# Kernel tuning notes

Measured on AMD Instinct MI355X. Metric: run time of the kernel, lower is better.

Reference implementation:

```python
import jax, jax.numpy as jnp
import numpy as np

T = 1.0  # temperature

def _free_energy(v, W, b, c):
    # v: [B, V]; W: [V, H]; b: [V]; c: [H]
    vW = v @ W                                  # [B, H]
    W_colsum = W.sum(axis=0)                    # [H]
    negF_normal = (v * b).sum(-1) - jax.nn.softplus(vW + c).sum(-1)
    negF_flip = ((1.0 - v) * b).sum(-1) - jax.nn.softplus(W_colsum - vW + c).sum(-1)
    negF = jnp.stack([negF_normal, negF_flip], axis=-1)  # [B, 2]
    return -T * jax.nn.logsumexp(negF / T, axis=-1)      # [B]

def _gibbs_chain(v0, W, b, c, key, k):
    B = v0.shape[0]
    key, k0 = jax.random.split(key)
    u0 = jax.random.bernoulli(k0, 0.5, (B, 1)).astype(v0.dtype)
    b_sum = b.sum()

    def step(carry, _):
        v, u, key = carry
        key, k1, k2, k3 = jax.random.split(key, 4)
        v_branch = u * v + (1.0 - u) * (1.0 - v)
        h = jax.random.bernoulli(k1, jax.nn.sigmoid(v_branch @ W + c)).astype(v.dtype)  # [B,H]
        a = h @ W.T                                                                     # [B,V]
        vb = (v * b).sum(-1)
        va = (v * a).sum(-1)
        dE = -b_sum - a.sum(-1) + 2.0 * vb + 2.0 * va
        u_new = jax.random.bernoulli(k2, jax.nn.sigmoid(dE)).astype(v.dtype)[:, None]
        v_new = jax.random.bernoulli(k3, jax.nn.sigmoid(a + b)).astype(v.dtype)
        v = u_new * v_new + (1.0 - u_new) * (1.0 - v_new)
        return (v, u_new, key), None

    (v_model, _, _), _ = jax.lax.scan(step, (v0, u0, key), None, length=k)
    return v_model

def setup_inputs() -> dict:
    key = jax.random.key(0)
    kv, kw = jax.random.split(key)
    B, V, H = 8192, 1024, 1024
    v_data = jnp.round(jax.random.uniform(kv, (B, V), dtype=jnp.float32))  # binary 0/1
    W = 0.01 * jax.random.normal(kw, (V, H), dtype=jnp.float32)
    b = jnp.zeros((V,), dtype=jnp.float32)
    c = jnp.zeros((H,), dtype=jnp.float32)
    return {"v_data": v_data, "W": W, "b": b, "c": c, "seed": 0}

def reference(v_data, W, b, c, seed):
    K = 10  # Gibbs steps
    key = jax.random.key(seed)
    v_model = _gibbs_chain(v_data, W, b, c, key, K)
    v_model = jax.lax.stop_gradient(v_model)  # .detach() in torch
    loss = _free_energy(v_data, W, b, c).mean() - _free_energy(v_model, W, b, c).mean()
    return loss
```

## Files before the change

kernel.cpp:

```cpp
#include <hip/hip_runtime.h>
#include <hip/hip_bf16.h>
#include <stdint.h>
#include <math.h>


static constexpr int Bn = 8192;
static constexpr int Vn = 1024;
static constexpr int Hn = 1024;
static constexpr int KSTEPS = 10;

typedef _Float16 f16;
typedef f16   f16x4 __attribute__((ext_vector_type(4)));
typedef f16   f16x8 __attribute__((ext_vector_type(8)));
typedef float f32x4 __attribute__((ext_vector_type(4)));

#define GLOBAL_LOAD_LDS16(g, l)                                              \
  __builtin_amdgcn_global_load_lds(                                          \
      (const __attribute__((address_space(1))) uint32_t*)(g),                \
      (__attribute__((address_space(3))) uint32_t*)(l), 16, 0, 0)

__device__ __forceinline__ uint32_t rotl32(uint32_t x, int d) {
  return (x << d) | (x >> (32 - d));
}

__device__ __forceinline__ void tf2x32(uint32_t k0, uint32_t k1,
                                       uint32_t x0, uint32_t x1,
                                       uint32_t& o0, uint32_t& o1) {
  uint32_t k2 = k0 ^ k1 ^ 0x1BD11BDAu;
#define TFR(r) { x0 += x1; x1 = rotl32(x1, (r)); x1 ^= x0; }
  x0 += k0; x1 += k1;
  TFR(13) TFR(15) TFR(26) TFR(6)
  x0 += k1; x1 += k2 + 1u;
  TFR(17) TFR(29) TFR(16) TFR(24)
  x0 += k2; x1 += k0 + 2u;
  TFR(13) TFR(15) TFR(26) TFR(6)
  x0 += k0; x1 += k1 + 3u;
  TFR(17) TFR(29) TFR(16) TFR(24)
  x0 += k1; x1 += k2 + 4u;
  TFR(13) TFR(15) TFR(26) TFR(6)
  x0 += k2; x1 += k0 + 5u;
#undef TFR
  o0 = x0; o1 = x1;
}

__device__ __forceinline__ float rng_u01(uint2 key, uint32_t idx) {
  uint32_t o0, o1;
  tf2x32(key.x, key.y, 0u, idx, o0, o1);
  uint32_t bits = o0 ^ o1;
  return __uint_as_float((bits >> 9) | 0x3F800000u) - 1.0f;
}

__device__ __attribute__((noinline)) float4 rng4_u01(uint2 key, uint32_t i0,
                                                     uint32_t i1, uint32_t i2,
                                                     uint32_t i3) {
  float4 r;
  r.x = rng_u01(key, i0);
  r.y = rng_u01(key, i1);
  r.z = rng_u01(key, i2);
  r.w = rng_u01(key, i3);
  return r;
}

__device__ __forceinline__ float bern_fast(float z, float r01) {
  float e = __expf(-z);
  return (__builtin_fmaf(r01, e, r01) < 1.0f) ? 1.f : 0.f;
}
__device__ __forceinline__ float softplus_fast(float x) {
  return fmaxf(x, 0.f) + __logf(1.f + __expf(-fabsf(x)));
}

__global__ void prep_keys(const int* __restrict__ seedp, uint2* __restrict__ keys) {
  if (threadIdx.x != 0 || blockIdx.x != 0) return;
  uint32_t seed = (uint32_t)(*seedp);
  uint2 key = make_uint2(0u, seed);
  uint2 nk, kk;
  tf2x32(key.x, key.y, 0u, 0u, nk.x, nk.y);
  tf2x32(key.x, key.y, 0u, 1u, kk.x, kk.y);
  keys[0] = kk;
  key = nk;
  for (int s = 0; s < KSTEPS; ++s) {
    uint2 t0, t1, t2, t3;
    tf2x32(key.x, key.y, 0u, 0u, t0.x, t0.y);
    tf2x32(key.x, key.y, 0u, 1u, t1.x, t1.y);
    tf2x32(key.x, key.y, 0u, 2u, t2.x, t2.y);
    tf2x32(key.x, key.y, 0u, 3u, t3.x, t3.y);
    key = t0;
    keys[1 + 3*s] = t1;
    keys[2 + 3*s] = t2;
    keys[3 + 3*s] = t3;
  }
}

__global__ __launch_bounds__(256) void colsum_part(
    const float* __restrict__ W, float* __restrict__ part) {
  const int bx = blockIdx.x, t = threadIdx.x;
  float s0 = 0.f, s1 = 0.f, s2 = 0.f, s3 = 0.f;
#pragma unroll
  for (int r = 0; r < 16; ++r) {
    const float* row = W + (size_t)(bx * 16 + r) * Hn;
    s0 += row[t]; s1 += row[t + 256]; s2 += row[t + 512]; s3 += row[t + 768];
  }
  float* p = part + (size_t)bx * Hn;
  p[t] = s0; p[t + 256] = s1; p[t + 512] = s2; p[t + 768] = s3;
}

__global__ __launch_bounds__(256) void colsum_red(
    const float* __restrict__ part, float* __restrict__ cs) {
  const int col = blockIdx.x * 256 + threadIdx.x;
  float s = 0.f;
#pragma unroll
  for (int k = 0; k < 64; ++k) s += part[(size_t)k * Hn + col];
  cs[col] = s;
}

__global__ void bsum_k(const float* __restrict__ bvec, float* __restrict__ bs) {
  __shared__ float sb[4];
  float s = 0.f;
  for (int i = threadIdx.x; i < Vn; i += 256) s += bvec[i];
  for (int off = 32; off > 0; off >>= 1) s += __shfl_down(s, off, 64);
  int wv = threadIdx.x >> 6, ln = threadIdx.x & 63;
  if (ln == 0) sb[wv] = s;
  __syncthreads();
  if (threadIdx.x == 0) bs[0] = sb[0] + sb[1] + sb[2] + sb[3];
}

__global__ __launch_bounds__(256) void cast_W(
    const float* __restrict__ W, f16* __restrict__ Wf, f16* __restrict__ WTf) {
  __shared__ f16 tile[64][65];
  const int j0 = blockIdx.x * 64, i0 = blockIdx.y * 64;
  const int tx = threadIdx.x & 63, tg = threadIdx.x >> 6;
#pragma unroll 4
  for (int rr = 0; rr < 16; ++rr) {
    const int row = tg * 16 + rr;
    float w = W[(size_t)(i0 + row) * Hn + j0 + tx];
    f16 hw = (f16)w;
    Wf[(size_t)(i0 + row) * Hn + j0 + tx] = hw;
    tile[row][tx] = hw;
  }
  __syncthreads();
#pragma unroll 4
  for (int rr = 0; rr < 16; ++rr) {
    const int row = tg * 16 + rr;
    WTf[(size_t)(j0 + row) * Vn + i0 + tx] = tile[tx][row];
  }
}

__global__ void u0_init(const uint2* __restrict__ keys, float* __restrict__ u0) {
  int b = blockIdx.x * 256 + threadIdx.x;
  float r01 = rng_u01(keys[0], (uint32_t)b);
  u0[b] = (r01 < 0.5f) ? 1.f : 0.f;
}

__global__ __launch_bounds__(256) void cast_vx(
    const float* __restrict__ vd, const float* __restrict__ u0,
    const float* __restrict__ bvec, f16* __restrict__ x,
    float* __restrict__ pXB0) {
  const int row = blockIdx.x;
  const int t = threadIdx.x;
  const float uo = u0[row];
  const float4 d  = ((const float4*)(vd + (size_t)row * Vn))[t];
  const float4 bv = ((const float4*)bvec)[t];
  float xv[4] = { d.x, d.y, d.z, d.w };
  if (uo <= 0.5f) { xv[0]=1.f-xv[0]; xv[1]=1.f-xv[1]; xv[2]=1.f-xv[2]; xv[3]=1.f-xv[3]; }
  f16x4 o = { (f16)xv[0], (f16)xv[1], (f16)xv[2], (f16)xv[3] };
  *(f16x4*)(x + (size_t)row * Vn + t * 4) = o;
  float xb = xv[0]*bv.x + xv[1]*bv.y + xv[2]*bv.z + xv[3]*bv.w;
#pragma unroll
  for (int m = 1; m < 8; m <<= 1) xb += __shfl_xor(xb, m, 64);
  if ((t & 7) == 0) pXB0[(size_t)row * 32 + (t >> 3)] = xb;
}

template <int EPI>
__global__ __launch_bounds__(256, 2) void gemm_s(
    const f16* __restrict__ A, const f16* __restrict__ Bm,
    f16* __restrict__ outH, f16* __restrict__ xnew,
    const float* __restrict__ bvec, const float* __restrict__ cvec,
    const float* __restrict__ colsum,
    float* __restrict__ pA, float* __restrict__ pXA, float* __restrict__ pXBn,
    float* __restrict__ pSA, float* __restrict__ pSB,
    const uint2* __restrict__ keys, int keyIdx)
{
  constexpr int N = 1024, K = 1024, BK = 64;
  __shared__ alignas(16) f16 As[128 * BK];
  __shared__ alignas(16) f16 Bs[128 * BK];

  const int t = threadIdx.x, wave = t >> 6, lane = t & 63;
  const int l15 = lane & 15, quad = lane >> 4;
  const int m0 = blockIdx.x * 128, n0 = blockIdx.y * 128;
  const int wm = (wave >> 1) * 64, wn = (wave & 1) * 64;

  const int rbase = lane >> 3;
  const int gch   = (lane & 7) ^ rbase;
  const f16* gA = A  + (size_t)(m0 + wave * 32 + rbase) * K + gch * 8;
  const f16* gB = Bm + (size_t)(n0 + wave * 32 + rbase) * K + gch * 8;
  f16* lA = As + wave * 32 * BK;
  f16* lB = Bs + wave * 32 * BK;

  const int swz = l15 & 7;
  const int oA  = (wm + l15) * BK;
  const int oB  = (wn + l15) * BK;

  uint2 key = make_uint2(0u, 0u);
  if constexpr (EPI != 4) key = keys[keyIdx];

  f32x4 acc[4][4] = {};
  float r01v[64];

#pragma unroll 16
  for (int ki = 0; ki < 16; ++ki) {
    const int k0 = ki * 64;
#pragma unroll
    for (int i = 0; i < 4; ++i) {
      GLOBAL_LOAD_LDS16(gA + k0 + i * 8 * K, lA + i * 8 * BK);
      GLOBAL_LOAD_LDS16(gB + k0 + i * 8 * K, lB + i * 8 * BK);
    }
    if constexpr (EPI != 4) {
      uint32_t idx[4];
#pragma unroll
      for (int j = 0; j < 4; ++j) {
        const int e  = ki * 4 + j;
        const int mt = e >> 4, r = (e >> 2) & 3, nt = e & 3;
        const int gm = m0 + wm + mt * 16 + quad * 4 + r;
        const int gn = n0 + wn + nt * 16 + l15;
        idx[j] = (uint32_t)(gm * N + gn);
      }
      float4 rv = rng4_u01(key, idx[0], idx[1], idx[2], idx[3]);
      r01v[ki * 4 + 0] = rv.x;
      r01v[ki * 4 + 1] = rv.y;
      r01v[ki * 4 + 2] = rv.z;
      r01v[ki * 4 + 3] = rv.w;
    }
    __syncthreads();

#pragma unroll
    for (int kc = 0; kc < 2; ++kc) {
      const int fc = ((kc * 4 + quad) ^ swz) * 8;
      f16x8 af[4], bf[4];
#pragma unroll
      for (int i = 0; i < 4; ++i) {
        af[i] = *(const f16x8*)(&As[oA + i * 16 * BK + fc]);
        bf[i] = *(const f16x8*)(&Bs[oB + i * 16 * BK + fc]);
      }
#pragma unroll
      for (int mt = 0; mt < 4; ++mt)
#pragma unroll
        for (int nt = 0; nt < 4; ++nt)
          acc[mt][nt] = __builtin_amdgcn_mfma_f32_16x16x32_f16(af[mt], bf[nt], acc[mt][nt], 0, 0, 0);
    }
    __syncthreads();
  }

  const int slotBase = blockIdx.y * 4 + (wave & 1) * 2;

  if constexpr (EPI == 1 || EPI == 2) {
    float csv[4], cvv[4];
#pragma unroll
    for (int nt = 0; nt < 4; ++nt) {
      const int gn = n0 + wn + nt * 16 + l15;
      csv[nt] = colsum[gn];
      cvv[nt] = cvec[gn];
    }
#pragma unroll
    for (int mt = 0; mt < 4; ++mt)
#pragma unroll
      for (int r = 0; r < 4; ++r) {
        const int gm = m0 + wm + mt * 16 + quad * 4 + r;
#pragma unroll
        for (int p = 0; p < 2; ++p) {
          float pa = 0.f, pxa = 0.f, sa = 0.f, sb = 0.f;
#pragma unroll
          for (int q = 0; q < 2; ++q) {
            const int nt = p * 2 + q;
            const int gn = n0 + wn + nt * 16 + l15;
            const float val = acc[mt][nt][r];
            const float r01 = r01v[mt * 16 + r * 4 + nt];
            float hq  = bern_fast(val + cvv[nt], r01);
            outH[(size_t)gm * N + gn] = (f16)hq;
            pa  += hq * csv[nt];
            pxa += hq * val;
            if constexpr (EPI == 2) {
              sa += softplus_fast(val + cvv[nt]);
              sb += softplus_fast(csv[nt] - val + cvv[nt]);
            }
          }
#pragma unroll
          for (int m = 1; m < 16; m <<= 1) {
            pa  += __shfl_xor(pa,  m, 64);
            pxa += __shfl_xor(pxa, m, 64);
            if constexpr (EPI == 2) {
              sa += __shfl_xor(sa, m, 64);
              sb += __shfl_xor(sb, m, 64);
            }
          }
          if (l15 == 0) {
            pA [(size_t)gm * 32 + slotBase + p] = pa;
            pXA[(size_t)gm * 32 + slotBase + p] = pxa;
            if constexpr (EPI == 2) {
              pSA[(size_t)gm * 32 + slotBase + p] = sa;
              pSB[(size_t)gm * 32 + slotBase + p] = sb;
            }
          }
        }
      }
  } else if constexpr (EPI == 3) {
    float bb[4];
#pragma unroll
    for (int nt = 0; nt < 4; ++nt) bb[nt] = bvec[n0 + wn + nt * 16 + l15];
#pragma unroll
    for (int mt = 0; mt < 4; ++mt)
#pragma unroll
      for (int r = 0; r < 4; ++r) {
        const int gm = m0 + wm + mt * 16 + quad * 4 + r;
#pragma unroll
        for (int p = 0; p < 2; ++p) {
          float pxb = 0.f;
#pragma unroll
          for (int q = 0; q < 2; ++q) {
            const int nt = p * 2 + q;
            const int gn = n0 + wn + nt * 16 + l15;
            const float aval = acc[mt][nt][r];
            const float r01 = r01v[mt * 16 + r * 4 + nt];
            float xq  = bern_fast(aval + bb[nt], r01);
            xnew[(size_t)gm * N + gn] = (f16)xq;
            pxb += xq * bb[nt];
          }
#pragma unroll
          for (int m = 1; m < 16; m <<= 1) pxb += __shfl_xor(pxb, m, 64);
          if (l15 == 0) pXBn[(size_t)gm * 32 + slotBase + p] = pxb;
        }
      }
  } else {
    float csv[4], cvv[4];
#pragma unroll
    for (int nt = 0; nt < 4; ++nt) {
      const int gn = n0 + wn + nt * 16 + l15;
      csv[nt] = colsum[gn];
      cvv[nt] = cvec[gn];
    }
#pragma unroll
    for (int mt = 0; mt < 4; ++mt)
#pragma unroll
      for (int r = 0; r < 4; ++r) {
        const int gm = m0 + wm + mt * 16 + quad * 4 + r;
#pragma unroll
        for (int p = 0; p < 2; ++p) {
          float sa = 0.f, sb = 0.f;
#pragma unroll
          for (int q = 0; q < 2; ++q) {
            const int nt = p * 2 + q;
            const float val = acc[mt][nt][r];
            sa += softplus_fast(val + cvv[nt]);
            sb += softplus_fast(csv[nt] - val + cvv[nt]);
          }
#pragma unroll
          for (int m = 1; m < 16; m <<= 1) {
            sa += __shfl_xor(sa, m, 64);
            sb += __shfl_xor(sb, m, 64);
          }
          if (l15 == 0) {
            pSA[(size_t)gm * 32 + slotBase + p] = sa;
            pSB[(size_t)gm * 32 + slotBase + p] = sb;
          }
        }
      }
  }
}

__global__ __launch_bounds__(256) void u_chain(
    const float* __restrict__ pA, const float* __restrict__ pXA,
    const float* __restrict__ pXB, const float* __restrict__ bsum,
    const uint2* __restrict__ keys, const float* __restrict__ u0,
    float* __restrict__ uF)
{
  const int t = threadIdx.x, wave = t >> 6, lane = t & 63;
  const int r2 = lane >> 5, slot = lane & 31;
  const int row = blockIdx.x * 8 + wave * 2 + r2;
  const float bs = bsum[0];
  float uo = u0[row];
  for (int s = 0; s < KSTEPS; ++s) {
    const size_t o = (size_t)s * 32 * Bn + (size_t)row * 32 + slot;
    float sa  = pA [o];
    float sxa = pXA[o];
    float sxb = pXB[o];
#pragma unroll
    for (int m = 1; m < 32; m <<= 1) {
      sa  += __shfl_xor(sa,  m, 64);
      sxa += __shfl_xor(sxa, m, 64);
      sxb += __shfl_xor(sxb, m, 64);
    }
    const float va = (uo > 0.5f) ? sxa : sa - sxa;
    const float vb = (uo > 0.5f) ? sxb : bs - sxb;
    const float dE = -bs - sa + 2.f * vb + 2.f * va;
    uo = bern_fast(dE, rng_u01(keys[2 + 3 * s], (uint32_t)row));
  }
  if (slot == 0) uF[row] = uo;
}

__device__ __forceinline__ float fe_eval(float SA, float SB, float xb,
                                         float uo, float bs) {
  float S1 = (uo > 0.5f) ? SA : SB;
  float S2 = (uo > 0.5f) ? SB : SA;
  float vb = (uo > 0.5f) ? xb : bs - xb;
  float negn = vb - S1;
  float negf = (bs - vb) - S2;
  float mx = fmaxf(negn, negf);
  return -(mx + logf(expf(negn - mx) + expf(negf - mx)));
}

__global__ __launch_bounds__(256) void fe_finish(
    const float* __restrict__ SA0, const float* __restrict__ SB0,
    const float* __restrict__ xb0,
    const float* __restrict__ SAF, const float* __restrict__ SBF,
    const float* __restrict__ xbF,
    const float* __restrict__ u0, const float* __restrict__ uF,
    const float* __restrict__ bsum,
    float* __restrict__ Fd, float* __restrict__ Fm)
{
  const int t = threadIdx.x, wave = t >> 6, lane = t & 63;
  const int r2 = lane >> 5, slot = lane & 31;
  const int row = blockIdx.x * 8 + wave * 2 + r2;
  const size_t o = (size_t)row * 32 + slot;
  const float bs = bsum[0];
  float a0 = SA0[o], b0 = SB0[o], x0 = xb0[o];
  float aF = SAF[o], bF = SBF[o], xF = xbF[o];
#pragma unroll
  for (int m = 1; m < 32; m <<= 1) {
    a0 += __shfl_xor(a0, m, 64);  b0 += __shfl_xor(b0, m, 64);
    x0 += __shfl_xor(x0, m, 64);  aF += __shfl_xor(aF, m, 64);
    bF += __shfl_xor(bF, m, 64);  xF += __shfl_xor(xF, m, 64);
  }
  if (slot == 0) {
    Fd[row] = fe_eval(a0, b0, x0, u0[row], bs);
    Fm[row] = fe_eval(aF, bF, xF, uF[row], bs);
  }
}

__global__ __launch_bounds__(256) void finalize_k(
    const float* __restrict__ Fd, const float* __restrict__ Fm, float* __restrict__ out)
{
  __shared__ double sb[8];
  double sd = 0.0, sm = 0.0;
  for (int i = threadIdx.x; i < Bn; i += 256) { sd += (double)Fd[i]; sm += (double)Fm[i]; }
  for (int off = 32; off > 0; off >>= 1) { sd += __shfl_down(sd, off, 64); sm += __shfl_down(sm, off, 64); }
  const int wv = threadIdx.x >> 6, ln = threadIdx.x & 63;
  if (ln == 0) { sb[wv] = sd; sb[4 + wv] = sm; }
  __syncthreads();
  if (threadIdx.x == 0) {
    sd = sb[0] + sb[1] + sb[2] + sb[3];
    sm = sb[4] + sb[5] + sb[6] + sb[7];
    out[0] = (float)((sd - sm) / (double)Bn);
  }
}

extern "C" void kernel_launch(void* const* d_in, const int* in_sizes, int n_in,
                              void* d_out, int out_size, void* d_ws, size_t ws_size,
                              hipStream_t stream) {
  const float* v_data = (const float*)d_in[0];
  const float* W      = (const float*)d_in[1];
  const float* bvec   = (const float*)d_in[2];
  const float* cvec   = (const float*)d_in[3];
  const int*   seedp  = (const int*)d_in[4];
  float* out = (float*)d_out;

  char* ws = (char*)d_ws;
  size_t off = 0;
  auto alloc = [&](size_t bytes) -> void* {
    void* p = ws + off;
    off += (bytes + 255) & ~(size_t)255;
    return p;
  };
  f16*   xb0  = (f16*)alloc((size_t)Bn * Vn * 2);
  f16*   xb1  = (f16*)alloc((size_t)Bn * Vn * 2);
  f16*   h    = (f16*)alloc((size_t)Bn * Hn * 2);
  f16*   Wf   = (f16*)alloc((size_t)Vn * Hn * 2);
  f16*   WTf  = (f16*)alloc((size_t)Vn * Hn * 2);
  float* cpart  = (float*)alloc(64 * Hn * 4);
  float* colsum = (float*)alloc(Hn * 4);
  float* bsum   = (float*)alloc(256);
  uint2* keys   = (uint2*)alloc(64 * sizeof(uint2));
  float* u0     = (float*)alloc(Bn * 4);
  float* uF     = (float*)alloc(Bn * 4);
  float* pA     = (float*)alloc((size_t)KSTEPS * 32 * Bn * 4);
  float* pXA    = (float*)alloc((size_t)KSTEPS * 32 * Bn * 4);
  float* pXB    = (float*)alloc((size_t)(KSTEPS + 1) * 32 * Bn * 4);
  float* SA0    = (float*)alloc((size_t)32 * Bn * 4);
  float* SB0    = (float*)alloc((size_t)32 * Bn * 4);
  float* SAF    = (float*)alloc((size_t)32 * Bn * 4);
  float* SBF    = (float*)alloc((size_t)32 * Bn * 4);
  float* Fd     = (float*)alloc(Bn * 4);
  float* Fm     = (float*)alloc(Bn * 4);
  (void)ws_size; (void)in_sizes; (void)n_in; (void)out_size;

  prep_keys<<<1, 64, 0, stream>>>(seedp, keys);
  colsum_part<<<64, 256, 0, stream>>>(W, cpart);
  colsum_red<<<4, 256, 0, stream>>>(cpart, colsum);
  bsum_k<<<1, 256, 0, stream>>>(bvec, bsum);
  cast_W<<<dim3(Hn / 64, Vn / 64), 256, 0, stream>>>(W, Wf, WTf);
  u0_init<<<Bn / 256, 256, 0, stream>>>(keys, u0);
  cast_vx<<<Bn, 256, 0, stream>>>(v_data, u0, bvec, xb0, pXB);

  dim3 gg(Bn / 128, Hn / 128);
  f16* xs[2] = { xb0, xb1 };
  const size_t SL = (size_t)32 * Bn;

  for (int s = 0; s < KSTEPS; ++s) {
    if (s == 0) {
      gemm_s<2><<<gg, 256, 0, stream>>>(xs[0], WTf, h, nullptr, nullptr, cvec,
                                        colsum, pA, pXA, nullptr, SA0, SB0,
                                        keys, 1);
    } else {
      gemm_s<1><<<gg, 256, 0, stream>>>(xs[s & 1], WTf, h, nullptr, nullptr, cvec,
                                        colsum, pA + (size_t)s * SL,
                                        pXA + (size_t)s * SL, nullptr,
                                        nullptr, nullptr, keys, 1 + 3 * s);
    }
    gemm_s<3><<<gg, 256, 0, stream>>>(h, Wf, nullptr, xs[(s + 1) & 1], bvec,
                                      nullptr, nullptr, nullptr, nullptr,
                                      pXB + (size_t)(s + 1) * SL,
                                      nullptr, nullptr, keys, 3 + 3 * s);
  }

  gemm_s<4><<<gg, 256, 0, stream>>>(xs[KSTEPS & 1], WTf, nullptr, nullptr,
                                    nullptr, cvec, colsum, nullptr, nullptr,
                                    nullptr, SAF, SBF, keys, 0);

  u_chain<<<Bn / 8, 256, 0, stream>>>(pA, pXA, pXB, bsum, keys, u0, uF);
  fe_finish<<<Bn / 8, 256, 0, stream>>>(SA0, SB0, pXB,
                                        SAF, SBF, pXB + (size_t)KSTEPS * SL,
                                        u0, uF, bsum, Fd, Fm);
  finalize_k<<<1, 256, 0, stream>>>(Fd, Fm, out);
}
```

Measured before the change: 950.6 us.

## Double-buffer LDS tiles in GEMM to overlap global loads with MFMA

Splits the shared-memory A/B tiles into two buffers and prefetches the next K-slice via global_load_lds while MFMAs consume the current one. This cuts the per-iteration pair of barriers to one and hides global-to-LDS latency. LDS usage doubles to 64KB per block, which at two blocks per CU may reduce occupancy. The loop is now fully unrolled with per-iteration buffer selection.

```diff
diff --git a/kernel.cpp b/kernel.cpp
--- a/kernel.cpp
+++ b/kernel.cpp
@@ -181,8 +181,8 @@
     const uint2* __restrict__ keys, int keyIdx)
 {
   constexpr int N = 1024, K = 1024, BK = 64;
-  __shared__ alignas(16) f16 As[128 * BK];
-  __shared__ alignas(16) f16 Bs[128 * BK];
+  __shared__ alignas(16) f16 As[2][128 * BK];
+  __shared__ alignas(16) f16 Bs[2][128 * BK];
 
   const int t = threadIdx.x, wave = t >> 6, lane = t & 63;
   const int l15 = lane & 15, quad = lane >> 4;
@@ -193,8 +193,7 @@
   const int gch   = (lane & 7) ^ rbase;
   const f16* gA = A  + (size_t)(m0 + wave * 32 + rbase) * K + gch * 8;
   const f16* gB = Bm + (size_t)(n0 + wave * 32 + rbase) * K + gch * 8;
-  f16* lA = As + wave * 32 * BK;
-  f16* lB = Bs + wave * 32 * BK;
+  const int woff = wave * 32 * BK;
 
   const int swz = l15 & 7;
   const int oA  = (wm + l15) * BK;
@@ -206,13 +205,25 @@
   f32x4 acc[4][4] = {};
   float r01v[64];
 
-#pragma unroll 16
+#pragma unroll
+  for (int i = 0; i < 4; ++i) {
+    GLOBAL_LOAD_LDS16(gA + i * 8 * K, As[0] + woff + i * 8 * BK);
+    GLOBAL_LOAD_LDS16(gB + i * 8 * K, Bs[0] + woff + i * 8 * BK);
+  }
+  __syncthreads();
+
+#pragma unroll
   for (int ki = 0; ki < 16; ++ki) {
-    const int k0 = ki * 64;
-#pragma unroll
-    for (int i = 0; i < 4; ++i) {
-      GLOBAL_LOAD_LDS16(gA + k0 + i * 8 * K, lA + i * 8 * BK);
-      GLOBAL_LOAD_LDS16(gB + k0 + i * 8 * K, lB + i * 8 * BK);
+    const int cur = ki & 1;
+    if (ki < 15) {
+      const int k0n = (ki + 1) * 64;
+      f16* wA = (cur ? As[0] : As[1]) + woff;
+      f16* wB = (cur ? Bs[0] : Bs[1]) + woff;
+#pragma unroll
+      for (int i = 0; i < 4; ++i) {
+        GLOBAL_LOAD_LDS16(gA + k0n + i * 8 * K, wA + i * 8 * BK);
+        GLOBAL_LOAD_LDS16(gB + k0n + i * 8 * K, wB + i * 8 * BK);
+      }
     }
     if constexpr (EPI != 4) {
       uint32_t idx[4];
@@ -230,16 +241,16 @@
       r01v[ki * 4 + 2] = rv.z;
       r01v[ki * 4 + 3] = rv.w;
     }
-    __syncthreads();
-
+    const f16* rA = cur ? As[1] : As[0];
+    const f16* rB = cur ? Bs[1] : Bs[0];
 #pragma unroll
     for (int kc = 0; kc < 2; ++kc) {
       const int fc = ((kc * 4 + quad) ^ swz) * 8;
       f16x8 af[4], bf[4];
 #pragma unroll
       for (int i = 0; i < 4; ++i) {
-        af[i] = *(const f16x8*)(&As[oA + i * 16 * BK + fc]);
-        bf[i] = *(const f16x8*)(&Bs[oB + i * 16 * BK + fc]);
+        af[i] = *(const f16x8*)(&rA[oA + i * 16 * BK + fc]);
+        bf[i] = *(const f16x8*)(&rB[oB + i * 16 * BK + fc]);
       }
 #pragma unroll
       for (int mt = 0; mt < 4; ++mt)
@@ -247,7 +258,7 @@
         for (int nt = 0; nt < 4; ++nt)
           acc[mt][nt] = __builtin_amdgcn_mfma_f32_16x16x32_f16(af[mt], bf[nt], acc[mt][nt], 0, 0, 0);
     }
-    __syncthreads();
+    if (ki < 15) __syncthreads();
   }
 
   const int slotBase = blockIdx.y * 4 + (wave & 1) * 2;
```

New measurement: 947.7 us. No clear change (-0.3%).
